# Kernel tuning notes

Measured on AMD Instinct MI355X. Metric: run time of the kernel, lower is better.

Reference implementation:

```python
import jax, jax.numpy as jnp
import numpy as np

TEMPERATURE = 1.0  # module's set_temperature value; mode=False path: out = x + attn_out * temperature


def setup_inputs() -> dict:
    key = jax.random.key(0)
    ks = jax.random.split(key, 7)
    B, C, H, W = 4, 256, 64, 64
    Cqk = C // 8
    s = 0.02
    return {
        "x": jax.random.normal(ks[0], (B, C, H, W), dtype=jnp.float32),
        "Wq": jax.random.normal(ks[1], (Cqk, C), dtype=jnp.float32) * s,
        "bq": jax.random.normal(ks[2], (Cqk,), dtype=jnp.float32) * s,
        "Wk": jax.random.normal(ks[3], (Cqk, C), dtype=jnp.float32) * s,
        "bk": jax.random.normal(ks[4], (Cqk,), dtype=jnp.float32) * s,
        "Wv": jax.random.normal(ks[5], (C, C), dtype=jnp.float32) * s,
        "bv": jax.random.normal(ks[6], (C,), dtype=jnp.float32) * s,
    }


def reference(x, Wq, bq, Wk, bk, Wv, bv):
    B, C, H, W = x.shape
    N = H * W
    xf = x.reshape(B, C, N)                      # flatten spatial -> tokens
    # 1x1 convs == pointwise linear over channels
    q = jnp.einsum('oc,bcn->bno', Wq, xf) + bq            # [B, N, Cqk]
    k = jnp.einsum('oc,bcn->bon', Wk, xf) + bk[:, None]   # [B, Cqk, N]
    attn = jax.nn.softmax(jnp.einsum('bno,bom->bnm', q, k), axis=-1)  # [B, N, N]
    v = jnp.einsum('oc,bcn->bon', Wv, xf) + bv[:, None]   # [B, C, N]
    # torch: bmm(value, attn^T) -> out[b,c,m] = sum_n v[b,c,n] * attn[b,m,n]
    out = jnp.einsum('bcn,bmn->bcm', v, attn).reshape(B, C, H, W)
    return x + out * TEMPERATURE
```

## Files before the change

### kernel.cpp

```cpp
#include <hip/hip_runtime.h>

#define BATCH 4
#define CH    256
#define NTOK  4096
#define DQK   32

typedef __attribute__((ext_vector_type(4))) float  f32x4;
typedef __attribute__((ext_vector_type(2))) float  f32x2;
typedef __attribute__((ext_vector_type(8))) __bf16 bf16x8;
typedef __attribute__((ext_vector_type(2))) unsigned int u32x2;
typedef __attribute__((ext_vector_type(4))) unsigned int u32x4;

static __device__ __forceinline__ unsigned short f2bf(float f) {
    unsigned int u = __builtin_bit_cast(unsigned int, f);
    unsigned int r = u + 0x7FFFu + ((u >> 16) & 1u);
    return (unsigned short)(r >> 16);
}
static __device__ __forceinline__ unsigned int pack2(float a, float b) {
    return (unsigned int)f2bf(a) | ((unsigned int)f2bf(b) << 16);
}

__global__ __launch_bounds__(256)
void wconv(const float* __restrict__ Wq, const float* __restrict__ Wk,
           const float* __restrict__ Wv, unsigned short* __restrict__ Wbf,
           unsigned int* __restrict__ Mk)
{
    if (blockIdx.x == 0 && threadIdx.x < BATCH) Mk[threadIdx.x] = 0u;
    const int id = (blockIdx.x * 256 + threadIdx.x) * 4;
    const int r  = id >> 8;
    const int c  = id & 255;
    const float* src = (r < 32) ? (Wq + r * 256 + c)
                     : (r < 64) ? (Wk + (r - 32) * 256 + c)
                                : (Wv + (size_t)(r - 64) * 256 + c);
    float v0 = src[0], v1 = src[1], v2 = src[2], v3 = src[3];
    u32x2 p = {pack2(v0, v1), pack2(v2, v3)};
    *reinterpret_cast<u32x2*>(Wbf + id) = p;
}

__global__ __launch_bounds__(256, 4)
void qkv_proj(const float* __restrict__ x,
              const float* __restrict__ pbq, const float* __restrict__ pbk,
              const float* __restrict__ pbv,
              const unsigned short* __restrict__ Wbf,
              unsigned short* __restrict__ Qh,
              unsigned short* __restrict__ Kh,
              unsigned short* __restrict__ Vh,
              unsigned int* __restrict__ Mk)
{
    const int t    = threadIdx.x;
    const int wave = t >> 6;
    const int lane = t & 63;
    const int low  = lane & 15;
    const int quad = lane >> 4;
    const int tok0 = blockIdx.x * 16;
    const int b    = tok0 >> 12;
    const int nl0  = tok0 & (NTOK - 1);

    __shared__ unsigned short sm[16 * 264];
    __shared__ unsigned short ob[256 * 24];

    {
        const int c64 = t >> 2;
        const int t4  = (t & 3) * 4;
        #pragma unroll
        for (int cg = 0; cg < 4; ++cg) {
            const int row = cg * 64 + c64;
            const f32x4 v = *reinterpret_cast<const f32x4*>(
                x + ((size_t)b * CH + row) * NTOK + nl0 + t4);
            #pragma unroll
            for (int j = 0; j < 4; ++j)
                sm[(t4 + j) * 264 + row] = f2bf(v[j]);
        }
    }

    f32x4 acc[5];
    #pragma unroll
    for (int j = 0; j < 5; ++j) {
        const int rtg = wave * 5 + j;
        float bb = (rtg < 2) ? pbq[rtg * 16 + low]
                 : (rtg < 4) ? pbk[(rtg - 2) * 16 + low]
                             : pbv[(rtg - 4) * 16 + low];
        f32x4 z = {bb, bb, bb, bb};
        acc[j] = z;
    }
    __syncthreads();

    #pragma unroll
    for (int k0 = 0; k0 < 8; ++k0) {
        const bf16x8 af = *reinterpret_cast<const bf16x8*>(
            sm + low * 264 + k0 * 32 + quad * 8);
        #pragma unroll
        for (int j = 0; j < 5; ++j) {
            const int rtg = wave * 5 + j;
            const bf16x8 bf = *reinterpret_cast<const bf16x8*>(
                Wbf + (size_t)(rtg * 16 + low) * 256 + k0 * 32 + quad * 8);
            acc[j] = __builtin_amdgcn_mfma_f32_16x16x32_bf16(af, bf, acc[j], 0, 0, 0);
        }
    }

    #pragma unroll
    for (int j = 0; j < 5; ++j) {
        const int rtg = wave * 5 + j;
        if (rtg < 4) {
            unsigned short* dst = (rtg < 2) ? Qh : Kh;
            const int wr = (rtg & 1) * 16 + low;
            #pragma unroll
            for (int reg = 0; reg < 4; ++reg) {
                const int token = tok0 + quad * 4 + reg;
                dst[(size_t)token * DQK + wr] = f2bf(acc[j][reg]);
            }
        }
    }
    if (wave == 0) {
        f32x4 kk = acc[2] * acc[2] + acc[3] * acc[3];
        #pragma unroll
        for (int mask = 1; mask <= 8; mask <<= 1)
            #pragma unroll
            for (int reg = 0; reg < 4; ++reg)
                kk[reg] += __shfl_xor(kk[reg], mask);
        if (low == 0) {
            #pragma unroll
            for (int reg = 0; reg < 4; ++reg)
                atomicMax(&Mk[b], __builtin_bit_cast(unsigned int, kk[reg]));
        }
    }

    #pragma unroll
    for (int j = 0; j < 5; ++j) {
        const int rtg = wave * 5 + j;
        if (rtg >= 4) {
            const int c = (rtg - 4) * 16 + low;
            #pragma unroll
            for (int reg = 0; reg < 4; ++reg)
                ob[c * 24 + quad * 4 + reg] = f2bf(acc[j][reg]);
        }
    }
    __syncthreads();
    {
        const unsigned int* obd = (const unsigned int*)ob;
        const int h = t & 1;
        #pragma unroll
        for (int pass = 0; pass < 2; ++pass) {
            const int c = (t >> 1) + pass * 128;
            const u32x4 v = *reinterpret_cast<const u32x4*>(obd + c * 12 + h * 4);
            *reinterpret_cast<u32x4*>(
                Vh + ((size_t)b * CH + c) * NTOK + nl0 + h * 8) = v;
        }
    }
}

__global__ __launch_bounds__(512, 2)
void attn(const float* __restrict__ x,
          const unsigned short* __restrict__ Qh,
          const unsigned short* __restrict__ Kh,
          const unsigned short* __restrict__ Vh,
          const unsigned int* __restrict__ Mk,
          float* __restrict__ out)
{
    const int t    = threadIdx.x;
    const int wave = t >> 6;
    const int kg   = wave & 3;
    const int ch   = wave >> 2;
    const int lane = t & 63;
    const int low  = lane & 15;
    const int quad = lane >> 4;

    const int beta = blockIdx.x;
    const int b    = (beta & 7) >> 1;
    const int q0   = (((beta >> 3) * 2) + (beta & 1)) * 64;

    __shared__ float smem[11264 + 256];
    unsigned int*   Pdw = (unsigned int*)smem;
    unsigned short* Ph  = (unsigned short*)smem;
    float* lbuf = smem + 11264;

    const float LOG2E = 1.44269504088896f;

    bf16x8 qfrag[2];
    float  m2[2];
    {
        const float M2 = __builtin_bit_cast(float, Mk[b]);
        #pragma unroll
        for (int j = 0; j < 2; ++j) {
            const int qs = 2 * ch + j;
            qfrag[j] = *reinterpret_cast<const bf16x8*>(
                Qh + (size_t)(b * NTOK + q0 + qs * 16 + low) * DQK + quad * 8);
            float qn2 = 0.f;
            #pragma unroll
            for (int e = 0; e < 8; ++e) {
                float qv = (float)qfrag[j][e];
                qn2 += qv * qv;
            }
            qn2 += __shfl_xor(qn2, 16);
            qn2 += __shfl_xor(qn2, 32);
            m2[j] = __builtin_sqrtf(qn2 * M2) * (1.02f * LOG2E);
        }
    }

    f32x4 acc[4][8];
    #pragma unroll
    for (int qs = 0; qs < 4; ++qs)
        #pragma unroll
        for (int ct = 0; ct < 8; ++ct) { f32x4 z = {0.f,0.f,0.f,0.f}; acc[qs][ct] = z; }
    float l_s[2] = {0.f, 0.f};

    const unsigned short* Kb = Kh + (size_t)b * NTOK * DQK;
    const unsigned short* Vb = Vh + (size_t)b * CH * NTOK;

    bf16x8 kf[4];
    #pragma unroll
    for (int kt = 0; kt < 4; ++kt)
        kf[kt] = *reinterpret_cast<const bf16x8*>(
            Kb + (size_t)(kg * 64 + kt * 16 + low) * DQK + quad * 8);

    for (int i = 0; i < 16; ++i) {
        const int n0 = (i * 4 + kg) * 64;
        const int n1 = (((i + 1) & 15) * 4 + kg) * 64;

        #pragma unroll
        for (int j = 0; j < 2; ++j) {
            const int qs = 2 * ch + j;
            f32x4 S[4];
            #pragma unroll
            for (int kt = 0; kt < 4; ++kt) {
                f32x4 z = {0.f,0.f,0.f,0.f};
                S[kt] = __builtin_amdgcn_mfma_f32_16x16x32_bf16(kf[kt], qfrag[j], z, 0, 0, 0);
            }
            float sum = 0.f;
            unsigned int* pq = Pdw + kg * 2816 + (qs * 16 + low) * 44 + quad * 2;
            #pragma unroll
            for (int kt = 0; kt < 4; ++kt) {
                float p0 = __builtin_amdgcn_exp2f(S[kt][0] * LOG2E - m2[j]);
                float p1 = __builtin_amdgcn_exp2f(S[kt][1] * LOG2E - m2[j]);
                float p2 = __builtin_amdgcn_exp2f(S[kt][2] * LOG2E - m2[j]);
                float p3 = __builtin_amdgcn_exp2f(S[kt][3] * LOG2E - m2[j]);
                sum += (p0 + p1) + (p2 + p3);
                u32x2 w2 = {pack2(p0, p1), pack2(p2, p3)};
                *reinterpret_cast<u32x2*>(pq + kt * 8) = w2;
            }
            l_s[j] += sum;
        }

        bf16x8 kn[4];
        #pragma unroll
        for (int kt = 0; kt < 4; ++kt)
            kn[kt] = *reinterpret_cast<const bf16x8*>(
                Kb + (size_t)(n1 + kt * 16 + low) * DQK + quad * 8);

        __syncthreads();

        #pragma unroll
        for (int s = 0; s < 2; ++s) {
            bf16x8 pf[4];
            #pragma unroll
            for (int qs = 0; qs < 4; ++qs)
                pf[qs] = *reinterpret_cast<const bf16x8*>(
                    Ph + kg * 5632 + (qs * 16 + low) * 88 + s * 32 + quad * 8);
            #pragma unroll
            for (int ct = 0; ct < 8; ++ct) {
                const bf16x8 vf = *reinterpret_cast<const bf16x8*>(
                    Vb + (size_t)(ch * 128 + ct * 16 + low) * NTOK + n0 + s * 32 + quad * 8);
                #pragma unroll
                for (int qs = 0; qs < 4; ++qs)
                    acc[qs][ct] = __builtin_amdgcn_mfma_f32_16x16x32_bf16(vf, pf[qs], acc[qs][ct], 0, 0, 0);
            }
        }

        __syncthreads();

        #pragma unroll
        for (int kt = 0; kt < 4; ++kt) kf[kt] = kn[kt];
    }

    #pragma unroll
    for (int j = 0; j < 2; ++j) {
        l_s[j] += __shfl_xor(l_s[j], 16);
        l_s[j] += __shfl_xor(l_s[j], 32);
    }
    if (quad == 0) {
        #pragma unroll
        for (int j = 0; j < 2; ++j)
            lbuf[kg * 64 + (2 * ch + j) * 16 + low] = l_s[j];
    }

    const int q = t & 63;
    const int u = t >> 6;
    float invl = 0.f;
    for (int rd = 0; rd < 8; ++rd) {
        #pragma unroll
        for (int qs = 0; qs < 4; ++qs) {
            float* sl = smem + wave * 1408 + (qs * 16 + low) * 22 + quad * 4;
            f32x2 lo = {acc[qs][rd][0], acc[qs][rd][1]};
            f32x2 hi = {acc[qs][rd][2], acc[qs][rd][3]};
            *reinterpret_cast<f32x2*>(sl)     = lo;
            *reinterpret_cast<f32x2*>(sl + 2) = hi;
        }
        __syncthreads();
        if (rd == 0)
            invl = 1.0f / (((lbuf[q] + lbuf[64 + q]) + (lbuf[128 + q] + lbuf[192 + q])));

        #pragma unroll
        for (int p = 0; p < 4; ++p) {
            const int half = p >> 1;
            const int c15  = u * 2 + (p & 1);
            const int wb   = half * 4;
            float O = (smem[(wb + 0) * 1408 + q * 22 + c15]
                     + smem[(wb + 1) * 1408 + q * 22 + c15])
                    + (smem[(wb + 2) * 1408 + q * 22 + c15]
                     + smem[(wb + 3) * 1408 + q * 22 + c15]);
            const int c = half * 128 + rd * 16 + c15;
            const size_t idx = (size_t)(b * CH + c) * NTOK + q0 + q;
            out[idx] = x[idx] + O * invl;
        }
        __syncthreads();
    }
}

extern "C" void kernel_launch(void* const* d_in, const int* in_sizes, int n_in,
                              void* d_out, int out_size, void* d_ws, size_t ws_size,
                              hipStream_t stream) {
    const float* x  = (const float*)d_in[0];
    const float* Wq = (const float*)d_in[1];
    const float* bq = (const float*)d_in[2];
    const float* Wk = (const float*)d_in[3];
    const float* bk = (const float*)d_in[4];
    const float* Wv = (const float*)d_in[5];
    const float* bv = (const float*)d_in[6];
    float* out = (float*)d_out;

    unsigned short* Qh  = (unsigned short*)d_ws;
    unsigned short* Kh  = Qh  + (size_t)BATCH * NTOK * DQK;
    unsigned short* Vh  = Kh  + (size_t)BATCH * NTOK * DQK;
    unsigned short* Wbf = Vh  + (size_t)BATCH * CH * NTOK;
    unsigned int*   Mk  = (unsigned int*)(Wbf + 320 * 256);

    wconv<<<dim3(80), dim3(256), 0, stream>>>(Wq, Wk, Wv, Wbf, Mk);
    qkv_proj<<<dim3(1024), dim3(256), 0, stream>>>(x, bq, bk, bv, Wbf,
                                                   Qh, Kh, Vh, Mk);
    attn<<<dim3(256), dim3(512), 0, stream>>>(x, Qh, Kh, Vh, Mk, out);
}
```

Baseline: 244.7 us.

## Double-buffer P tiles in LDS and load x fragments directly in projection

The attention kernel now keeps two LDS buffers for the probability tile. It computes the next iteration's QK scores and exponentials before the PV MFMAs on the current buffer, which removes one barrier per iteration and overlaps the two phases. The row padding of the P layout changes from 44 to 36 dwords, and total LDS use grows. Separately, the projection kernel drops its LDS staging of x and gathers each bf16 fragment straight from global memory with strided scalar loads. That removes a barrier but risks uncoalesced reads.

```diff
diff --git a/kernel.cpp b/kernel.cpp
--- a/kernel.cpp
+++ b/kernel.cpp
@@ -56,22 +56,7 @@
     const int b    = tok0 >> 12;
     const int nl0  = tok0 & (NTOK - 1);
 
-    __shared__ unsigned short sm[16 * 264];
     __shared__ unsigned short ob[256 * 24];
-
-    {
-        const int c64 = t >> 2;
-        const int t4  = (t & 3) * 4;
-        #pragma unroll
-        for (int cg = 0; cg < 4; ++cg) {
-            const int row = cg * 64 + c64;
-            const f32x4 v = *reinterpret_cast<const f32x4*>(
-                x + ((size_t)b * CH + row) * NTOK + nl0 + t4);
-            #pragma unroll
-            for (int j = 0; j < 4; ++j)
-                sm[(t4 + j) * 264 + row] = f2bf(v[j]);
-        }
-    }
 
     f32x4 acc[5];
     #pragma unroll
@@ -83,12 +68,19 @@
         f32x4 z = {bb, bb, bb, bb};
         acc[j] = z;
     }
-    __syncthreads();
+
+    const float* xb = x + (size_t)b * CH * NTOK + nl0 + low;
 
     #pragma unroll
     for (int k0 = 0; k0 < 8; ++k0) {
-        const bf16x8 af = *reinterpret_cast<const bf16x8*>(
-            sm + low * 264 + k0 * 32 + quad * 8);
+        const int cbase = k0 * 32 + quad * 8;
+        float xv[8];
+        #pragma unroll
+        for (int e = 0; e < 8; ++e)
+            xv[e] = xb[(size_t)(cbase + e) * NTOK];
+        u32x4 ap = {pack2(xv[0], xv[1]), pack2(xv[2], xv[3]),
+                    pack2(xv[4], xv[5]), pack2(xv[6], xv[7])};
+        const bf16x8 af = __builtin_bit_cast(bf16x8, ap);
         #pragma unroll
         for (int j = 0; j < 5; ++j) {
             const int rtg = wave * 5 + j;
@@ -169,10 +161,9 @@
     const int b    = (beta & 7) >> 1;
     const int q0   = (((beta >> 3) * 2) + (beta & 1)) * 64;
 
-    __shared__ float smem[11264 + 256];
-    unsigned int*   Pdw = (unsigned int*)smem;
-    unsigned short* Ph  = (unsigned short*)smem;
-    float* lbuf = smem + 11264;
+    __shared__ float smem[18432 + 256];
+    unsigned int* Pbase = (unsigned int*)smem;
+    float* lbuf = smem + 18432;
 
     const float LOG2E = 1.44269504088896f;
 
@@ -207,70 +198,73 @@
     const unsigned short* Kb = Kh + (size_t)b * NTOK * DQK;
     const unsigned short* Vb = Vh + (size_t)b * CH * NTOK;
 
-    bf16x8 kf[4];
-    #pragma unroll
-    for (int kt = 0; kt < 4; ++kt)
-        kf[kt] = *reinterpret_cast<const bf16x8*>(
-            Kb + (size_t)(kg * 64 + kt * 16 + low) * DQK + quad * 8);
+    #define S_PHASE(ii, buf)                                                    \
+    {                                                                           \
+        const int n0s = ((ii) * 4 + kg) * 64;                                   \
+        bf16x8 kf[4];                                                           \
+        _Pragma("unroll")                                                       \
+        for (int kt = 0; kt < 4; ++kt)                                          \
+            kf[kt] = *reinterpret_cast<const bf16x8*>(                          \
+                Kb + (size_t)(n0s + kt * 16 + low) * DQK + quad * 8);           \
+        _Pragma("unroll")                                                       \
+        for (int j = 0; j < 2; ++j) {                                           \
+            const int qs = 2 * ch + j;                                          \
+            f32x4 S[4];                                                         \
+            _Pragma("unroll")                                                   \
+            for (int kt = 0; kt < 4; ++kt) {                                    \
+                f32x4 z = {0.f,0.f,0.f,0.f};                                    \
+                S[kt] = __builtin_amdgcn_mfma_f32_16x16x32_bf16(kf[kt],         \
+                            qfrag[j], z, 0, 0, 0);                              \
+            }                                                                   \
+            float sum = 0.f;                                                    \
+            unsigned int* pq = Pbase + (buf) * 9216 + kg * 2304                 \
+                               + (qs * 16 + low) * 36 + quad * 2;               \
+            _Pragma("unroll")                                                   \
+            for (int kt = 0; kt < 4; ++kt) {                                    \
+                float p0 = __builtin_amdgcn_exp2f(S[kt][0] * LOG2E - m2[j]);    \
+                float p1 = __builtin_amdgcn_exp2f(S[kt][1] * LOG2E - m2[j]);    \
+                float p2 = __builtin_amdgcn_exp2f(S[kt][2] * LOG2E - m2[j]);    \
+                float p3 = __builtin_amdgcn_exp2f(S[kt][3] * LOG2E - m2[j]);    \
+                sum += (p0 + p1) + (p2 + p3);                                   \
+                u32x2 w2 = {pack2(p0, p1), pack2(p2, p3)};                      \
+                *reinterpret_cast<u32x2*>(pq + kt * 8) = w2;                    \
+            }                                                                   \
+            l_s[j] += sum;                                                      \
+        }                                                                       \
+    }
+
+    S_PHASE(0, 0)
 
     for (int i = 0; i < 16; ++i) {
-        const int n0 = (i * 4 + kg) * 64;
-        const int n1 = (((i + 1) & 15) * 4 + kg) * 64;
-
-        #pragma unroll
-        for (int j = 0; j < 2; ++j) {
-            const int qs = 2 * ch + j;
-            f32x4 S[4];
-            #pragma unroll
-            for (int kt = 0; kt < 4; ++kt) {
-                f32x4 z = {0.f,0.f,0.f,0.f};
-                S[kt] = __builtin_amdgcn_mfma_f32_16x16x32_bf16(kf[kt], qfrag[j], z, 0, 0, 0);
-            }
-            float sum = 0.f;
-            unsigned int* pq = Pdw + kg * 2816 + (qs * 16 + low) * 44 + quad * 2;
-            #pragma unroll
-            for (int kt = 0; kt < 4; ++kt) {
-                float p0 = __builtin_amdgcn_exp2f(S[kt][0] * LOG2E - m2[j]);
-                float p1 = __builtin_amdgcn_exp2f(S[kt][1] * LOG2E - m2[j]);
-                float p2 = __builtin_amdgcn_exp2f(S[kt][2] * LOG2E - m2[j]);
-                float p3 = __builtin_amdgcn_exp2f(S[kt][3] * LOG2E - m2[j]);
-                sum += (p0 + p1) + (p2 + p3);
-                u32x2 w2 = {pack2(p0, p1), pack2(p2, p3)};
-                *reinterpret_cast<u32x2*>(pq + kt * 8) = w2;
-            }
-            l_s[j] += sum;
-        }
-
-        bf16x8 kn[4];
-        #pragma unroll
-        for (int kt = 0; kt < 4; ++kt)
-            kn[kt] = *reinterpret_cast<const bf16x8*>(
-                Kb + (size_t)(n1 + kt * 16 + low) * DQK + quad * 8);
-
         __syncthreads();
 
-        #pragma unroll
-        for (int s = 0; s < 2; ++s) {
-            bf16x8 pf[4];
-            #pragma unroll
-            for (int qs = 0; qs < 4; ++qs)
-                pf[qs] = *reinterpret_cast<const bf16x8*>(
-                    Ph + kg * 5632 + (qs * 16 + low) * 88 + s * 32 + quad * 8);
-            #pragma unroll
-            for (int ct = 0; ct < 8; ++ct) {
-                const bf16x8 vf = *reinterpret_cast<const bf16x8*>(
-                    Vb + (size_t)(ch * 128 + ct * 16 + low) * NTOK + n0 + s * 32 + quad * 8);
+        if (i < 15) S_PHASE(i + 1, (i + 1) & 1)
+
+        {
+            const int n0 = (i * 4 + kg) * 64;
+            const unsigned short* Phh =
+                (const unsigned short*)(Pbase + (i & 1) * 9216);
+            #pragma unroll
+            for (int s = 0; s < 2; ++s) {
+                bf16x8 pf[4];
                 #pragma unroll
                 for (int qs = 0; qs < 4; ++qs)
-                    acc[qs][ct] = __builtin_amdgcn_mfma_f32_16x16x32_bf16(vf, pf[qs], acc[qs][ct], 0, 0, 0);
+                    pf[qs] = *reinterpret_cast<const bf16x8*>(
+                        Phh + kg * 4608 + (qs * 16 + low) * 72 + s * 32 + quad * 8);
+                #pragma unroll
+                for (int ct = 0; ct < 8; ++ct) {
+                    const bf16x8 vf = *reinterpret_cast<const bf16x8*>(
+                        Vb + (size_t)(ch * 128 + ct * 16 + low) * NTOK
+                           + n0 + s * 32 + quad * 8);
+                    #pragma unroll
+                    for (int qs = 0; qs < 4; ++qs)
+                        acc[qs][ct] = __builtin_amdgcn_mfma_f32_16x16x32_bf16(
+                            vf, pf[qs], acc[qs][ct], 0, 0, 0);
+                }
             }
         }
-
-        __syncthreads();
-
-        #pragma unroll
-        for (int kt = 0; kt < 4; ++kt) kf[kt] = kn[kt];
-    }
+    }
+    #undef S_PHASE
 
     #pragma unroll
     for (int j = 0; j < 2; ++j) {
```

Measured after the change: 243.8 us. No clear change (-0.4%).
